# Optimization experiments

Measured on AMD Instinct MI355X. Metric: run time of the kernel, lower is better.

Reference implementation:

```python
import jax, jax.numpy as jnp
import numpy as np

N_NODES = 65536
N_EDGES = 1048576
D_FEAT = 64
UNITS = 64


def setup_inputs() -> dict:
    key = jax.random.key(0)
    k1, k2, k3, k4, k5 = jax.random.split(key, 5)
    nodes = jax.random.normal(k1, (N_NODES, D_FEAT), dtype=jnp.float32)
    edge_vals = jax.random.uniform(k2, (N_EDGES,), dtype=jnp.float32)
    kernel = jax.random.normal(k3, (D_FEAT, UNITS), dtype=jnp.float32) * (1.0 / np.sqrt(D_FEAT))
    src_idx = jax.random.randint(k4, (N_EDGES,), 0, N_NODES, dtype=jnp.int32)
    dst_idx = jnp.sort(jax.random.randint(k5, (N_EDGES,), 0, N_NODES, dtype=jnp.int32))
    return {"nodes": nodes, "edge_vals": edge_vals, "kernel": kernel,
            "src_idx": src_idx, "dst_idx": dst_idx}


def reference(nodes, edge_vals, kernel, src_idx, dst_idx):
    # sparse_dense_matmul(A, X): for each edge (dst, src, w): agg[dst] += w * X[src]
    msgs = edge_vals[:, None] * nodes[src_idx]          # [E, d]
    agg = jax.ops.segment_sum(msgs, dst_idx, num_segments=nodes.shape[0])  # [N, d]
    # dense projection (activation is None -> linear)
    return agg @ kernel                                  # [N, units]
```

## Files before the change

### kernel.cpp

```cpp
#include <hip/hip_runtime.h>


constexpr int D = 64;
constexpr int EPW = 128;

__global__ __launch_bounds__(256) void zero_kernel(float4* __restrict__ p, int n4) {
    int i = blockIdx.x * blockDim.x + threadIdx.x;
    int stride = gridDim.x * blockDim.x;
    for (; i < n4; i += stride) p[i] = make_float4(0.f, 0.f, 0.f, 0.f);
}

__global__ __launch_bounds__(256) void gemm_nodes(const float* __restrict__ nodes,
                                                  const float* __restrict__ Km,
                                                  float* __restrict__ P, int n_nodes) {
    constexpr int S = 136;
    __shared__ float aT[D * S];
    __shared__ float Ks[D * D];
    const int t = threadIdx.x;
    const long R0 = (long)blockIdx.x * 128;

    for (int i = t; i < D * D / 4; i += 256)
        ((float4*)Ks)[i] = ((const float4*)Km)[i];

    {
        const int ro = t >> 4, c4 = (t & 15) * 4;
        #pragma unroll
        for (int r = 0; r < 8; ++r) {
            long row = R0 + r * 16 + ro;
            long lrow = row < n_nodes ? row : (long)(n_nodes - 1);
            float4 g = *(const float4*)&nodes[lrow * D + c4];
            int rl = r * 16 + ro;
            aT[(c4 + 0) * S + rl] = g.x;
            aT[(c4 + 1) * S + rl] = g.y;
            aT[(c4 + 2) * S + rl] = g.z;
            aT[(c4 + 3) * S + rl] = g.w;
        }
    }
    __syncthreads();

    const int tx = t & 15, ty = t >> 4;
    const int u0 = tx * 4, r0 = ty * 8;
    float4 acc[8];
    #pragma unroll
    for (int i = 0; i < 8; ++i) acc[i] = make_float4(0.f, 0.f, 0.f, 0.f);

    #pragma unroll 2
    for (int d = 0; d < D; ++d) {
        const float4 kk = *(const float4*)&Ks[d * D + u0];
        const float4 a0 = *(const float4*)&aT[d * S + r0];
        const float4 a1 = *(const float4*)&aT[d * S + r0 + 4];
        const float ar[8] = {a0.x, a0.y, a0.z, a0.w, a1.x, a1.y, a1.z, a1.w};
        #pragma unroll
        for (int i = 0; i < 8; ++i) {
            acc[i].x = fmaf(ar[i], kk.x, acc[i].x);
            acc[i].y = fmaf(ar[i], kk.y, acc[i].y);
            acc[i].z = fmaf(ar[i], kk.z, acc[i].z);
            acc[i].w = fmaf(ar[i], kk.w, acc[i].w);
        }
    }
    #pragma unroll
    for (int i = 0; i < 8; ++i) {
        long row = R0 + r0 + i;
        if (row < n_nodes) *(float4*)&P[row * D + u0] = acc[i];
    }
}

__global__ __launch_bounds__(256) void scatter_sorted(
    const float* __restrict__ P, const float* __restrict__ evals,
    const int* __restrict__ src, const int* __restrict__ dst,
    float* __restrict__ out, int n_edges)
{
    const int lane = threadIdx.x & 63;
    const int wid  = blockIdx.x * (blockDim.x >> 6) + (threadIdx.x >> 6);
    const long base = (long)wid * EPW;
    if (base >= n_edges) return;

    const int first = dst[base];
    int prev = first;
    float acc = 0.f;

    if (base + EPW <= n_edges) {
        #pragma unroll 1
        for (int i0 = 0; i0 < EPW; i0 += 16) {
            const int4*   sp = (const int4*)  &src[base + i0];
            const int4*   dp = (const int4*)  &dst[base + i0];
            const float4* wp = (const float4*)&evals[base + i0];
            const int4   sv0 = sp[0], sv1 = sp[1], sv2 = sp[2], sv3 = sp[3];
            const int4   dv0 = dp[0], dv1 = dp[1], dv2 = dp[2], dv3 = dp[3];
            const float4 wv0 = wp[0], wv1 = wp[1], wv2 = wp[2], wv3 = wp[3];

            float v[16];
            v[ 0] = P[(long)sv0.x * D + lane]; v[ 1] = P[(long)sv0.y * D + lane];
            v[ 2] = P[(long)sv0.z * D + lane]; v[ 3] = P[(long)sv0.w * D + lane];
            v[ 4] = P[(long)sv1.x * D + lane]; v[ 5] = P[(long)sv1.y * D + lane];
            v[ 6] = P[(long)sv1.z * D + lane]; v[ 7] = P[(long)sv1.w * D + lane];
            v[ 8] = P[(long)sv2.x * D + lane]; v[ 9] = P[(long)sv2.y * D + lane];
            v[10] = P[(long)sv2.z * D + lane]; v[11] = P[(long)sv2.w * D + lane];
            v[12] = P[(long)sv3.x * D + lane]; v[13] = P[(long)sv3.y * D + lane];
            v[14] = P[(long)sv3.z * D + lane]; v[15] = P[(long)sv3.w * D + lane];

            const int   dvs[16] = {dv0.x, dv0.y, dv0.z, dv0.w, dv1.x, dv1.y, dv1.z, dv1.w,
                                   dv2.x, dv2.y, dv2.z, dv2.w, dv3.x, dv3.y, dv3.z, dv3.w};
            const float wvs[16] = {wv0.x, wv0.y, wv0.z, wv0.w, wv1.x, wv1.y, wv1.z, wv1.w,
                                   wv2.x, wv2.y, wv2.z, wv2.w, wv3.x, wv3.y, wv3.z, wv3.w};
            #pragma unroll
            for (int k = 0; k < 16; ++k) {
                if (dvs[k] != prev) {
                    float* o = &out[(long)prev * D + lane];
                    if (prev == first) atomicAdd(o, acc);
                    else               *o = acc;
                    acc = 0.f;
                    prev = dvs[k];
                }
                acc = fmaf(wvs[k], v[k], acc);
            }
        }
    } else {
        for (long e = base; e < n_edges; ++e) {
            int s = src[e], dc = dst[e]; float w = evals[e];
            float v = P[(long)s * D + lane];
            if (dc != prev) {
                float* o = &out[(long)prev * D + lane];
                if (prev == first) atomicAdd(o, acc);
                else               *o = acc;
                acc = 0.f;
                prev = dc;
            }
            acc = fmaf(w, v, acc);
        }
    }
    atomicAdd(&out[(long)prev * D + lane], acc);
}

__global__ __launch_bounds__(256) void project_inplace(float* __restrict__ out,
                                                       const float* __restrict__ Km, int n_nodes) {
    __shared__ float Ks[D * D];
    const int t = threadIdx.x;
    for (int i = t; i < D * D; i += 256) Ks[i] = Km[i];
    __syncthreads();
    const int lane = t & 63;
    const int n = blockIdx.x * 4 + (t >> 6);
    if (n >= n_nodes) return;
    float* row = out + (long)n * D;
    const float rv = row[lane];
    float acc = 0.f;
    #pragma unroll
    for (int d = 0; d < D; ++d) acc = fmaf(__shfl(rv, d), Ks[d * D + lane], acc);
    row[lane] = acc;
}

extern "C" void kernel_launch(void* const* d_in, const int* in_sizes, int n_in,
                              void* d_out, int out_size, void* d_ws, size_t ws_size,
                              hipStream_t stream) {
    const float* nodes = (const float*)d_in[0];
    const float* evals = (const float*)d_in[1];
    const float* Km    = (const float*)d_in[2];
    const int*   src   = (const int*)d_in[3];
    const int*   dst   = (const int*)d_in[4];
    float* out = (float*)d_out;

    const int n_nodes = in_sizes[0] / D;
    const int n_edges = in_sizes[1];
    const int n_waves = (n_edges + EPW - 1) / EPW;

    zero_kernel<<<2048, 256, 0, stream>>>((float4*)out, out_size / 4);

    const size_t need = (size_t)n_nodes * D * sizeof(float);
    if (ws_size >= need) {
        float* P = (float*)d_ws;
        gemm_nodes<<<(n_nodes + 127) / 128, 256, 0, stream>>>(nodes, Km, P, n_nodes);
        scatter_sorted<<<(n_waves + 3) / 4, 256, 0, stream>>>(P, evals, src, dst, out, n_edges);
    } else {
        scatter_sorted<<<(n_waves + 3) / 4, 256, 0, stream>>>(nodes, evals, src, dst, out, n_edges);
        project_inplace<<<(n_nodes + 3) / 4, 256, 0, stream>>>(out, Km, n_nodes);
    }
}
```

Before: 132.3 us.

## Store projected node features in bf16 to halve gather traffic

The node-projection GEMM now writes its output table in bf16 instead of fp32, and the scatter kernel is templated to gather bf16 values and widen them to float before accumulating. This halves the bytes read per random gather and shrinks the intermediate table so more of it can sit in cache. The GEMM is also restructured to read node rows directly from global memory, with no transposed shared-memory tile, and to write packed 16-byte rows. The cost is reduced precision in the projected features, which may exceed the accuracy tolerance.

```diff
diff --git a/kernel.cpp b/kernel.cpp
--- a/kernel.cpp
+++ b/kernel.cpp
@@ -1,4 +1,5 @@
 #include <hip/hip_runtime.h>
+#include <hip/hip_bf16.h>
 
 
 constexpr int D = 64;
@@ -10,63 +11,80 @@
     for (; i < n4; i += stride) p[i] = make_float4(0.f, 0.f, 0.f, 0.f);
 }
 
-__global__ __launch_bounds__(256) void gemm_nodes(const float* __restrict__ nodes,
-                                                  const float* __restrict__ Km,
-                                                  float* __restrict__ P, int n_nodes) {
-    constexpr int S = 136;
-    __shared__ float aT[D * S];
+__global__ __launch_bounds__(256) void gemm_nodes_bf16(const float* __restrict__ nodes,
+                                                       const float* __restrict__ Km,
+                                                       __hip_bfloat16* __restrict__ P,
+                                                       int n_nodes) {
     __shared__ float Ks[D * D];
     const int t = threadIdx.x;
-    const long R0 = (long)blockIdx.x * 128;
-
     for (int i = t; i < D * D / 4; i += 256)
         ((float4*)Ks)[i] = ((const float4*)Km)[i];
+    __syncthreads();
 
-    {
-        const int ro = t >> 4, c4 = (t & 15) * 4;
+    const int rx = t & 31, uy = t >> 5;
+    const long R0 = (long)blockIdx.x * 128 + rx * 4;
+    const int u0 = uy * 8;
+
+    float acc[4][8];
+    #pragma unroll
+    for (int i = 0; i < 4; ++i)
         #pragma unroll
-        for (int r = 0; r < 8; ++r) {
-            long row = R0 + r * 16 + ro;
-            long lrow = row < n_nodes ? row : (long)(n_nodes - 1);
-            float4 g = *(const float4*)&nodes[lrow * D + c4];
-            int rl = r * 16 + ro;
-            aT[(c4 + 0) * S + rl] = g.x;
-            aT[(c4 + 1) * S + rl] = g.y;
-            aT[(c4 + 2) * S + rl] = g.z;
-            aT[(c4 + 3) * S + rl] = g.w;
+        for (int j = 0; j < 8; ++j) acc[i][j] = 0.f;
+
+    #pragma unroll 4
+    for (int dq = 0; dq < 16; ++dq) {
+        float a_s[4][4];
+        #pragma unroll
+        for (int i = 0; i < 4; ++i) {
+            long row = R0 + i; if (row >= n_nodes) row = n_nodes - 1;
+            const float4 g = *(const float4*)&nodes[row * D + dq * 4];
+            a_s[i][0] = g.x; a_s[i][1] = g.y; a_s[i][2] = g.z; a_s[i][3] = g.w;
+        }
+        #pragma unroll
+        for (int di = 0; di < 4; ++di) {
+            const float4 k0 = *(const float4*)&Ks[(dq * 4 + di) * D + u0];
+            const float4 k1 = *(const float4*)&Ks[(dq * 4 + di) * D + u0 + 4];
+            const float kv[8] = {k0.x, k0.y, k0.z, k0.w, k1.x, k1.y, k1.z, k1.w};
+            #pragma unroll
+            for (int i = 0; i < 4; ++i)
+                #pragma unroll
+                for (int j = 0; j < 8; ++j)
+                    acc[i][j] = fmaf(a_s[i][di], kv[j], acc[i][j]);
         }
     }
-    __syncthreads();
 
-    const int tx = t & 15, ty = t >> 4;
-    const int u0 = tx * 4, r0 = ty * 8;
-    float4 acc[8];
     #pragma unroll
-    for (int i = 0; i < 8; ++i) acc[i] = make_float4(0.f, 0.f, 0.f, 0.f);
-
-    #pragma unroll 2
-    for (int d = 0; d < D; ++d) {
-        const float4 kk = *(const float4*)&Ks[d * D + u0];
-        const float4 a0 = *(const float4*)&aT[d * S + r0];
-        const float4 a1 = *(const float4*)&aT[d * S + r0 + 4];
-        const float ar[8] = {a0.x, a0.y, a0.z, a0.w, a1.x, a1.y, a1.z, a1.w};
-        #pragma unroll
-        for (int i = 0; i < 8; ++i) {
-            acc[i].x = fmaf(ar[i], kk.x, acc[i].x);
-            acc[i].y = fmaf(ar[i], kk.y, acc[i].y);
-            acc[i].z = fmaf(ar[i], kk.z, acc[i].z);
-            acc[i].w = fmaf(ar[i], kk.w, acc[i].w);
+    for (int i = 0; i < 4; ++i) {
+        long row = R0 + i;
+        if (row < n_nodes) {
+            ushort u[8];
+            #pragma unroll
+            for (int j = 0; j < 8; ++j) {
+                __hip_bfloat16 b = __float2bfloat16(acc[i][j]);
+                u[j] = *(ushort*)&b;
+            }
+            uint4 pk;
+            pk.x = (uint)u[0] | ((uint)u[1] << 16);
+            pk.y = (uint)u[2] | ((uint)u[3] << 16);
+            pk.z = (uint)u[4] | ((uint)u[5] << 16);
+            pk.w = (uint)u[6] | ((uint)u[7] << 16);
+            *(uint4*)&P[row * D + u0] = pk;
         }
-    }
-    #pragma unroll
-    for (int i = 0; i < 8; ++i) {
-        long row = R0 + r0 + i;
-        if (row < n_nodes) *(float4*)&P[row * D + u0] = acc[i];
     }
 }
 
+template <typename T>
+__device__ __forceinline__ float load_feat(const T* P, long idx);
+template <>
+__device__ __forceinline__ float load_feat<__hip_bfloat16>(const __hip_bfloat16* P, long idx) {
+    return __bfloat162float(P[idx]);
+}
+template <>
+__device__ __forceinline__ float load_feat<float>(const float* P, long idx) { return P[idx]; }
+
+template <typename T>
 __global__ __launch_bounds__(256) void scatter_sorted(
-    const float* __restrict__ P, const float* __restrict__ evals,
+    const T* __restrict__ P, const float* __restrict__ evals,
     const int* __restrict__ src, const int* __restrict__ dst,
     float* __restrict__ out, int n_edges)
 {
@@ -89,15 +107,11 @@
             const int4   dv0 = dp[0], dv1 = dp[1], dv2 = dp[2], dv3 = dp[3];
             const float4 wv0 = wp[0], wv1 = wp[1], wv2 = wp[2], wv3 = wp[3];
 
+            const int svs[16] = {sv0.x, sv0.y, sv0.z, sv0.w, sv1.x, sv1.y, sv1.z, sv1.w,
+                                 sv2.x, sv2.y, sv2.z, sv2.w, sv3.x, sv3.y, sv3.z, sv3.w};
             float v[16];
-            v[ 0] = P[(long)sv0.x * D + lane]; v[ 1] = P[(long)sv0.y * D + lane];
-            v[ 2] = P[(long)sv0.z * D + lane]; v[ 3] = P[(long)sv0.w * D + lane];
-            v[ 4] = P[(long)sv1.x * D + lane]; v[ 5] = P[(long)sv1.y * D + lane];
-            v[ 6] = P[(long)sv1.z * D + lane]; v[ 7] = P[(long)sv1.w * D + lane];
-            v[ 8] = P[(long)sv2.x * D + lane]; v[ 9] = P[(long)sv2.y * D + lane];
-            v[10] = P[(long)sv2.z * D + lane]; v[11] = P[(long)sv2.w * D + lane];
-            v[12] = P[(long)sv3.x * D + lane]; v[13] = P[(long)sv3.y * D + lane];
-            v[14] = P[(long)sv3.z * D + lane]; v[15] = P[(long)sv3.w * D + lane];
+            #pragma unroll
+            for (int k = 0; k < 16; ++k) v[k] = load_feat<T>(P, (long)svs[k] * D + lane);
 
             const int   dvs[16] = {dv0.x, dv0.y, dv0.z, dv0.w, dv1.x, dv1.y, dv1.z, dv1.w,
                                    dv2.x, dv2.y, dv2.z, dv2.w, dv3.x, dv3.y, dv3.z, dv3.w};
@@ -118,7 +132,7 @@
     } else {
         for (long e = base; e < n_edges; ++e) {
             int s = src[e], dc = dst[e]; float w = evals[e];
-            float v = P[(long)s * D + lane];
+            float v = load_feat<T>(P, (long)s * D + lane);
             if (dc != prev) {
                 float* o = &out[(long)prev * D + lane];
                 if (prev == first) atomicAdd(o, acc);
@@ -165,13 +179,15 @@
 
     zero_kernel<<<2048, 256, 0, stream>>>((float4*)out, out_size / 4);
 
-    const size_t need = (size_t)n_nodes * D * sizeof(float);
+    const size_t need = (size_t)n_nodes * D * sizeof(__hip_bfloat16);
     if (ws_size >= need) {
-        float* P = (float*)d_ws;
-        gemm_nodes<<<(n_nodes + 127) / 128, 256, 0, stream>>>(nodes, Km, P, n_nodes);
-        scatter_sorted<<<(n_waves + 3) / 4, 256, 0, stream>>>(P, evals, src, dst, out, n_edges);
+        __hip_bfloat16* P = (__hip_bfloat16*)d_ws;
+        gemm_nodes_bf16<<<(n_nodes + 127) / 128, 256, 0, stream>>>(nodes, Km, P, n_nodes);
+        scatter_sorted<__hip_bfloat16><<<(n_waves + 3) / 4, 256, 0, stream>>>(
+            P, evals, src, dst, out, n_edges);
     } else {
-        scatter_sorted<<<(n_waves + 3) / 4, 256, 0, stream>>>(nodes, evals, src, dst, out, n_edges);
+        scatter_sorted<float><<<(n_waves + 3) / 4, 256, 0, stream>>>(
+            nodes, evals, src, dst, out, n_edges);
         project_inplace<<<(n_nodes + 3) / 4, 256, 0, stream>>>(out, Km, n_nodes);
     }
 }
```

New measurement: 131.3 us. No clear change (-0.7%).
